# Performance work log

Hardware: AMD Instinct MI355X
Metric: run time of the kernel (lower is better)

Reference implementation:

```python
import jax, jax.numpy as jnp
import numpy as np

N_CLASSES_FG = 20  # n_classes - 1

def _norm(t, axis=1):
    # F.normalize(t, dim=axis, eps=1e-10)
    n = jnp.linalg.norm(t, axis=axis, keepdims=True)
    return t / jnp.maximum(n, 1e-10)

def setup_inputs() -> dict:
    key = jax.random.key(0)
    ks = jax.random.split(key, 6)
    B, C, H, W = 8, 512, 80, 80
    N, Hr, Wr = 100, 40, 40
    return {
        "code_C": jax.random.normal(ks[0], (B, C, H, W), jnp.float32),
        "code_BG": jax.random.normal(ks[1], (B, C, H, W), jnp.float32),
        "ref_code_c": jax.random.normal(ks[2], (N, C, Hr, Wr), jnp.float32),
        "ref_code_bg": jax.random.normal(ks[3], (N, C, Hr, Wr), jnp.float32),
        "sum_patch_coord": jax.random.randint(ks[4], (N, 2), 0, Hr, dtype=jnp.int32),
        "cls_mask": jax.random.randint(ks[5], (N,), 0, N_CLASSES_FG, dtype=jnp.int32),
    }

def reference(code_C, code_BG, ref_code_c, ref_code_bg, sum_patch_coord, cls_mask):
    B, Cdim, H, W = code_C.shape
    N = ref_code_c.shape[0]
    code_C = _norm(code_C)   # channelwise L2 normalize
    code_BG = _norm(code_BG)
    # gather per-annotation feature vectors: ref_code_c[i, :, pc[i,1], pc[i,0]] -> [N, C]
    code_vectors = ref_code_c[jnp.arange(N), :, sum_patch_coord[:, 1], sum_patch_coord[:, 0]]
    # mean-mode prototypes: class-wise mean of gathered vectors
    protos = jax.ops.segment_sum(code_vectors, cls_mask, num_segments=N_CLASSES_FG)  # [V, C]
    counts = jax.ops.segment_sum(jnp.ones((N,), code_vectors.dtype), cls_mask, num_segments=N_CLASSES_FG)
    protos = protos / jnp.maximum(counts, 1.0)[:, None]  # classes with 0 vectors stay zero
    # cosine-similarity maps against normalized prototypes
    prob_C = jnp.einsum('bchw,vc->bvhw', code_C, _norm(protos, axis=1))  # [B, V, H, W]
    # pick the most-background pixel (min of summed class similarity), k=1 topk(-x)
    flat = prob_C.sum(axis=1).reshape(B, -1)  # [B, H*W]
    idx = jnp.argmin(flat, axis=1)
    i_x, i_y = idx // W, idx % W
    min_vec = code_BG[jnp.arange(B), :, i_x, i_y]  # [B, C]
    prob_BG = jnp.einsum('bchw,bc->bhw', code_BG, min_vec)  # [B, H, W]
    probs = jnp.concatenate([prob_BG[:, None], prob_C], axis=1)  # [B, V+1, H, W]
    return jax.nn.softmax(probs, axis=1)
```

## Files before the change

kernel.cpp:

```cpp
#include <hip/hip_runtime.h>
#include <math.h>

#define BB 8
#define CC 512
#define HWSZ 6400
#define NN 100
#define HR 40
#define WR 40
#define VV 20
#define VO 21
#define TPX 128
#define NTILE (HWSZ / TPX)

typedef unsigned long long u64;

__device__ __forceinline__ unsigned mapf(float f) {
    unsigned b = __float_as_uint(f);
    return (b & 0x80000000u) ? ~b : (b | 0x80000000u);
}

__global__ __launch_bounds__(512) void k_protos(const float* __restrict__ refc,
                                                const int* __restrict__ coord,
                                                const int* __restrict__ cls,
                                                float* __restrict__ protosT,
                                                u64* __restrict__ batchMin) {
    const int v = blockIdx.x;
    const int c = threadIdx.x;
    if (v == 0 && c < BB) batchMin[c] = ~0ull;

    float acc = 0.f;
    int cnt = 0;
    for (int n = 0; n < NN; ++n) {
        if (cls[n] == v) {
            int y = coord[2 * n + 1];
            int x = coord[2 * n + 0];
            acc += refc[((size_t)(n * CC + c) * HR + y) * WR + x];
            ++cnt;
        }
    }
    acc /= fmaxf((float)cnt, 1.0f);

    float ss = acc * acc;
    #pragma unroll
    for (int off = 32; off; off >>= 1) ss += __shfl_xor(ss, off);
    __shared__ float sW[8];
    const int wave = c >> 6, lane = c & 63;
    if (lane == 0) sW[wave] = ss;
    __syncthreads();
    float tot = 0.f;
    #pragma unroll
    for (int w = 0; w < 8; ++w) tot += sW[w];
    float scale = 1.0f / fmaxf(sqrtf(tot), 1e-10f);

    protosT[c * VV + v] = acc * scale;
}

__global__ __launch_bounds__(256, 2) void k_probC(const float* __restrict__ codeC,
                                                  const float* __restrict__ protosT,
                                                  float* __restrict__ probC,
                                                  u64* __restrict__ batchMin) {
    __shared__ float red[4 * VO * TPX];
    __shared__ float sScale[TPX];
    __shared__ float sPart[2 * TPX];
    __shared__ u64 sKey[2];

    const int tid  = threadIdx.x;
    const int wave = tid >> 6, lane = tid & 63;
    const int b    = blockIdx.x / NTILE;
    const int tile = blockIdx.x % NTILE;
    const int c0   = __builtin_amdgcn_readfirstlane(wave * 128);

    const float* src = codeC + ((size_t)(b * CC + c0)) * HWSZ + tile * TPX + 2 * lane;
    const float* pt  = protosT + (size_t)c0 * VV;

    float2 d[VV];
    #pragma unroll
    for (int v = 0; v < VV; ++v) d[v] = make_float2(0.f, 0.f);
    float2 ss = make_float2(0.f, 0.f);

    #pragma unroll 8
    for (int c = 0; c < 128; ++c) {
        float2 x = *(const float2*)(src + (size_t)c * HWSZ);
        ss.x = fmaf(x.x, x.x, ss.x);
        ss.y = fmaf(x.y, x.y, ss.y);
        const float* pr = pt + c * VV;
        #pragma unroll
        for (int v = 0; v < VV; ++v) {
            float p = pr[v];
            d[v].x = fmaf(x.x, p, d[v].x);
            d[v].y = fmaf(x.y, p, d[v].y);
        }
    }

    #pragma unroll
    for (int v = 0; v < VV; ++v) {
        red[wave * (VO * TPX) + v * TPX + 2 * lane    ] = d[v].x;
        red[wave * (VO * TPX) + v * TPX + 2 * lane + 1] = d[v].y;
    }
    red[wave * (VO * TPX) + VV * TPX + 2 * lane    ] = ss.x;
    red[wave * (VO * TPX) + VV * TPX + 2 * lane + 1] = ss.y;
    __syncthreads();

    float psum = 0.f;
    for (int q = tid; q < VO * TPX; q += 256) {
        float t = red[q] + red[VO * TPX + q] + red[2 * VO * TPX + q] + red[3 * VO * TPX + q];
        red[q] = t;
        if (q < VV * TPX) psum += t;
    }
    __syncthreads();
    if (tid < TPX) sScale[tid] = 1.0f / fmaxf(sqrtf(red[VV * TPX + tid]), 1e-10f);
    sPart[(tid >> 7) * TPX + (tid & 127)] = psum;
    __syncthreads();

    float* dst = probC + (size_t)b * VV * HWSZ + tile * TPX;
    for (int q = tid; q < VV * TPX; q += 256) {
        int v = q >> 7, px = q & 127;
        dst[(size_t)v * HWSZ + px] = red[q] * sScale[px];
    }

    if (tid < TPX) {
        float total = (sPart[tid] + sPart[TPX + tid]) * sScale[tid];
        u64 key = ((u64)mapf(total) << 32) | (unsigned)(tile * TPX + tid);
        #pragma unroll
        for (int off = 32; off; off >>= 1) {
            u64 o = __shfl_xor(key, off);
            if (o < key) key = o;
        }
        if ((tid & 63) == 0) sKey[tid >> 6] = key;
    }
    __syncthreads();
    if (tid == 0) {
        u64 k = sKey[0] < sKey[1] ? sKey[0] : sKey[1];
        atomicMin(&batchMin[b], k);
    }
}

__global__ __launch_bounds__(512) void k_minvec(const u64* __restrict__ batchMin,
                                                const float* __restrict__ codeBG,
                                                float* __restrict__ minvecN) {
    const int b = blockIdx.x, c = threadIdx.x;
    const int pix = (int)(unsigned)(batchMin[b] & 0xFFFFFFFFull);
    float x = codeBG[(size_t)(b * CC + c) * HWSZ + pix];
    float ss = x * x;
    #pragma unroll
    for (int off = 32; off; off >>= 1) ss += __shfl_xor(ss, off);
    __shared__ float sW[8];
    if ((c & 63) == 0) sW[c >> 6] = ss;
    __syncthreads();
    float tot = 0.f;
    #pragma unroll
    for (int w = 0; w < 8; ++w) tot += sW[w];
    minvecN[b * CC + c] = x * (1.0f / fmaxf(sqrtf(tot), 1e-10f));
}

__global__ __launch_bounds__(256, 2) void k_bg_softmax(const float* __restrict__ codeBG,
                                                       const float* __restrict__ minvecN,
                                                       const float* __restrict__ probC,
                                                       float* __restrict__ out) {
    __shared__ float red2[4 * 2 * TPX];
    __shared__ float sExp[VO * TPX];
    __shared__ float sInv[TPX];

    const int tid  = threadIdx.x;
    const int wave = tid >> 6, lane = tid & 63;
    const int b    = blockIdx.x / NTILE;
    const int tile = blockIdx.x % NTILE;
    const int c0   = __builtin_amdgcn_readfirstlane(wave * 128);

    const float* src = codeBG + ((size_t)(b * CC + c0)) * HWSZ + tile * TPX + 2 * lane;
    const float* mv  = minvecN + b * CC + c0;

    float2 ss = make_float2(0.f, 0.f), dg = make_float2(0.f, 0.f);
    #pragma unroll 8
    for (int c = 0; c < 128; ++c) {
        float2 x = *(const float2*)(src + (size_t)c * HWSZ);
        float m = mv[c];
        ss.x = fmaf(x.x, x.x, ss.x);
        ss.y = fmaf(x.y, x.y, ss.y);
        dg.x = fmaf(x.x, m, dg.x);
        dg.y = fmaf(x.y, m, dg.y);
    }
    red2[wave * (2 * TPX) + 2 * lane    ] = ss.x;
    red2[wave * (2 * TPX) + 2 * lane + 1] = ss.y;
    red2[wave * (2 * TPX) + TPX + 2 * lane    ] = dg.x;
    red2[wave * (2 * TPX) + TPX + 2 * lane + 1] = dg.y;
    __syncthreads();
    {
        int q = tid;
        float t = red2[q] + red2[2 * TPX + q] + red2[4 * TPX + q] + red2[6 * TPX + q];
        red2[q] = t;
    }
    __syncthreads();

    if (tid < TPX) {
        const int px = tid;
        float pbg = red2[TPX + px] * (1.0f / fmaxf(sqrtf(red2[px]), 1e-10f));
        const float* pc = probC + (size_t)b * VV * HWSZ + tile * TPX + px;
        float pv[VO];
        pv[0] = pbg;
        #pragma unroll
        for (int v = 0; v < VV; ++v) pv[v + 1] = pc[(size_t)v * HWSZ];
        float m = pv[0];
        #pragma unroll
        for (int i = 1; i < VO; ++i) m = fmaxf(m, pv[i]);
        float se = 0.f;
        #pragma unroll
        for (int i = 0; i < VO; ++i) {
            float e = __expf(pv[i] - m);
            sExp[i * TPX + px] = e;
            se += e;
        }
        sInv[px] = 1.0f / se;
    }
    __syncthreads();

    float* dst = out + (size_t)b * VO * HWSZ + tile * TPX;
    for (int q = tid; q < VO * TPX; q += 256) {
        int v = q >> 7, px = q & 127;
        dst[(size_t)v * HWSZ + px] = sExp[q] * sInv[px];
    }
}

extern "C" void kernel_launch(void* const* d_in, const int* in_sizes, int n_in,
                              void* d_out, int out_size, void* d_ws, size_t ws_size,
                              hipStream_t stream) {
    const float* codeC  = (const float*)d_in[0];
    const float* codeBG = (const float*)d_in[1];
    const float* refc   = (const float*)d_in[2];
    const int* coord = (const int*)d_in[4];
    const int* cls   = (const int*)d_in[5];
    float* out = (float*)d_out;

    char* ws = (char*)d_ws;
    float* protosT  = (float*)(ws);
    float* probC    = (float*)(ws + 40960);
    float* minvecN  = (float*)(ws + 4136960);
    u64*   batchMin = (u64*)  (ws + 4153344);

    k_protos    <<<dim3(VV),        dim3(512), 0, stream>>>(refc, coord, cls, protosT, batchMin);
    k_probC     <<<dim3(BB * NTILE), dim3(256), 0, stream>>>(codeC, protosT, probC, batchMin);
    k_minvec    <<<dim3(BB),        dim3(512), 0, stream>>>(batchMin, codeBG, minvecN);
    k_bg_softmax<<<dim3(BB * NTILE), dim3(256), 0, stream>>>(codeBG, minvecN, probC, out);
}
```

Measured before the change: 71.07 us.

## Stage channel tiles via async global-to-LDS double buffering with wider pixel tiles

Both heavy kernels now stream input channel blocks of 32 into a double-buffered LDS stage using global_load_lds, prefetching the next block while computing on the current. The pixel tile grows to 256 so each thread handles four pixels with float4 reads. The reduction and softmax epilogues are reorganised so each thread owns a pixel and writes outputs directly. This halves the number of blocks to 200, which may leave CUs idle, and the larger LDS footprint limits occupancy.

New measurement: 91.17 us. 28.3% more time.

```diff
diff --git a/kernel.cpp b/kernel.cpp
--- a/kernel.cpp
+++ b/kernel.cpp
@@ -9,14 +9,22 @@
 #define WR 40
 #define VV 20
 #define VO 21
-#define TPX 128
-#define NTILE (HWSZ / TPX)
+#define TPX 256
+#define NT (HWSZ / TPX)
+#define KB 32
+#define NKB (CC / KB)
 
 typedef unsigned long long u64;
 
 __device__ __forceinline__ unsigned mapf(float f) {
     unsigned b = __float_as_uint(f);
     return (b & 0x80000000u) ? ~b : (b | 0x80000000u);
+}
+
+__device__ __forceinline__ void gload16(const float* gp, const float* lp) {
+    __builtin_amdgcn_global_load_lds(
+        (const __attribute__((address_space(1))) void*)gp,
+        (__attribute__((address_space(3))) void*)lp, 16, 0, 0);
 }
 
 __global__ __launch_bounds__(512) void k_protos(const float* __restrict__ refc,
@@ -59,79 +67,114 @@
                                                   const float* __restrict__ protosT,
                                                   float* __restrict__ probC,
                                                   u64* __restrict__ batchMin) {
-    __shared__ float red[4 * VO * TPX];
-    __shared__ float sScale[TPX];
-    __shared__ float sPart[2 * TPX];
-    __shared__ u64 sKey[2];
+    __shared__ float stage[2][KB * TPX];
+    __shared__ u64 sKey[4];
 
     const int tid  = threadIdx.x;
-    const int wave = tid >> 6, lane = tid & 63;
-    const int b    = blockIdx.x / NTILE;
-    const int tile = blockIdx.x % NTILE;
-    const int c0   = __builtin_amdgcn_readfirstlane(wave * 128);
-
-    const float* src = codeC + ((size_t)(b * CC + c0)) * HWSZ + tile * TPX + 2 * lane;
-    const float* pt  = protosT + (size_t)c0 * VV;
-
-    float2 d[VV];
-    #pragma unroll
-    for (int v = 0; v < VV; ++v) d[v] = make_float2(0.f, 0.f);
-    float2 ss = make_float2(0.f, 0.f);
-
-    #pragma unroll 8
-    for (int c = 0; c < 128; ++c) {
-        float2 x = *(const float2*)(src + (size_t)c * HWSZ);
-        ss.x = fmaf(x.x, x.x, ss.x);
-        ss.y = fmaf(x.y, x.y, ss.y);
-        const float* pr = pt + c * VV;
+    const int w    = tid >> 6, lane = tid & 63;
+    const int b    = blockIdx.x / NT;
+    const int tile = blockIdx.x % NT;
+    const int c0w  = __builtin_amdgcn_readfirstlane(w * 8);
+
+    const float* gbase = codeC + (size_t)b * CC * HWSZ + tile * TPX;
+
+    float d[VV][4];
+    #pragma unroll
+    for (int v = 0; v < VV; ++v) { d[v][0] = d[v][1] = d[v][2] = d[v][3] = 0.f; }
+    float ss0 = 0.f, ss1 = 0.f, ss2 = 0.f, ss3 = 0.f;
+
+    #pragma unroll
+    for (int k = 0; k < 8; ++k) {
+        int r = 4 * k + w;
+        gload16(gbase + (size_t)r * HWSZ + lane * 4, &stage[0][r * TPX]);
+    }
+    __syncthreads();
+
+    int buf = 0;
+    for (int t = 0; t < NKB; ++t) {
+        if (t < NKB - 1) {
+            #pragma unroll
+            for (int k = 0; k < 8; ++k) {
+                int r = 4 * k + w;
+                gload16(gbase + (size_t)((t + 1) * KB + r) * HWSZ + lane * 4,
+                        &stage[buf ^ 1][r * TPX]);
+            }
+        }
+        const float* pt = protosT + (size_t)(t * KB + c0w) * VV;
         #pragma unroll
-        for (int v = 0; v < VV; ++v) {
-            float p = pr[v];
-            d[v].x = fmaf(x.x, p, d[v].x);
-            d[v].y = fmaf(x.y, p, d[v].y);
-        }
-    }
-
-    #pragma unroll
-    for (int v = 0; v < VV; ++v) {
-        red[wave * (VO * TPX) + v * TPX + 2 * lane    ] = d[v].x;
-        red[wave * (VO * TPX) + v * TPX + 2 * lane + 1] = d[v].y;
-    }
-    red[wave * (VO * TPX) + VV * TPX + 2 * lane    ] = ss.x;
-    red[wave * (VO * TPX) + VV * TPX + 2 * lane + 1] = ss.y;
-    __syncthreads();
-
+        for (int j = 0; j < 8; ++j) {
+            float4 x = *(const float4*)&stage[buf][(w * 8 + j) * TPX + lane * 4];
+            ss0 = fmaf(x.x, x.x, ss0);
+            ss1 = fmaf(x.y, x.y, ss1);
+            ss2 = fmaf(x.z, x.z, ss2);
+            ss3 = fmaf(x.w, x.w, ss3);
+            const float* pr = pt + j * VV;
+            #pragma unroll
+            for (int v = 0; v < VV; ++v) {
+                float p = pr[v];
+                d[v][0] = fmaf(x.x, p, d[v][0]);
+                d[v][1] = fmaf(x.y, p, d[v][1]);
+                d[v][2] = fmaf(x.z, p, d[v][2]);
+                d[v][3] = fmaf(x.w, p, d[v][3]);
+            }
+        }
+        __syncthreads();
+        buf ^= 1;
+    }
+
+    float* redA = &stage[0][0];
+    const int px = tid;
+    float* dst = probC + (size_t)b * VV * HWSZ + tile * TPX;
+
+    *(float4*)&redA[(w * 11 + 0) * TPX + lane * 4] = make_float4(ss0, ss1, ss2, ss3);
+    #pragma unroll
+    for (int v = 0; v < 10; ++v)
+        *(float4*)&redA[(w * 11 + 1 + v) * TPX + lane * 4] =
+            make_float4(d[v][0], d[v][1], d[v][2], d[v][3]);
+    __syncthreads();
+
+    float ssT = redA[(0 * 11) * TPX + px] + redA[(1 * 11) * TPX + px] +
+                redA[(2 * 11) * TPX + px] + redA[(3 * 11) * TPX + px];
+    float scale = 1.0f / fmaxf(sqrtf(ssT), 1e-10f);
     float psum = 0.f;
-    for (int q = tid; q < VO * TPX; q += 256) {
-        float t = red[q] + red[VO * TPX + q] + red[2 * VO * TPX + q] + red[3 * VO * TPX + q];
-        red[q] = t;
-        if (q < VV * TPX) psum += t;
-    }
-    __syncthreads();
-    if (tid < TPX) sScale[tid] = 1.0f / fmaxf(sqrtf(red[VV * TPX + tid]), 1e-10f);
-    sPart[(tid >> 7) * TPX + (tid & 127)] = psum;
-    __syncthreads();
-
-    float* dst = probC + (size_t)b * VV * HWSZ + tile * TPX;
-    for (int q = tid; q < VV * TPX; q += 256) {
-        int v = q >> 7, px = q & 127;
-        dst[(size_t)v * HWSZ + px] = red[q] * sScale[px];
-    }
-
-    if (tid < TPX) {
-        float total = (sPart[tid] + sPart[TPX + tid]) * sScale[tid];
-        u64 key = ((u64)mapf(total) << 32) | (unsigned)(tile * TPX + tid);
-        #pragma unroll
-        for (int off = 32; off; off >>= 1) {
-            u64 o = __shfl_xor(key, off);
-            if (o < key) key = o;
-        }
-        if ((tid & 63) == 0) sKey[tid >> 6] = key;
-    }
+    #pragma unroll
+    for (int v = 0; v < 10; ++v) {
+        float dv = redA[(0 * 11 + 1 + v) * TPX + px] + redA[(1 * 11 + 1 + v) * TPX + px] +
+                   redA[(2 * 11 + 1 + v) * TPX + px] + redA[(3 * 11 + 1 + v) * TPX + px];
+        float p = dv * scale;
+        dst[(size_t)v * HWSZ + px] = p;
+        psum += p;
+    }
+    __syncthreads();
+
+    #pragma unroll
+    for (int v = 0; v < 10; ++v)
+        *(float4*)&redA[(w * 11 + v) * TPX + lane * 4] =
+            make_float4(d[10 + v][0], d[10 + v][1], d[10 + v][2], d[10 + v][3]);
+    __syncthreads();
+    #pragma unroll
+    for (int v = 0; v < 10; ++v) {
+        float dv = redA[(0 * 11 + v) * TPX + px] + redA[(1 * 11 + v) * TPX + px] +
+                   redA[(2 * 11 + v) * TPX + px] + redA[(3 * 11 + v) * TPX + px];
+        float p = dv * scale;
+        dst[(size_t)(10 + v) * HWSZ + px] = p;
+        psum += p;
+    }
+
+    u64 key = ((u64)mapf(psum) << 32) | (unsigned)(tile * TPX + px);
+    #pragma unroll
+    for (int off = 32; off; off >>= 1) {
+        u64 o = __shfl_xor(key, off);
+        if (o < key) key = o;
+    }
+    if (lane == 0) sKey[w] = key;
     __syncthreads();
     if (tid == 0) {
-        u64 k = sKey[0] < sKey[1] ? sKey[0] : sKey[1];
-        atomicMin(&batchMin[b], k);
+        u64 kk = sKey[0];
+        kk = sKey[1] < kk ? sKey[1] : kk;
+        kk = sKey[2] < kk ? sKey[2] : kk;
+        kk = sKey[3] < kk ? sKey[3] : kk;
+        atomicMin(&batchMin[b], kk);
     }
 }
 
@@ -157,68 +200,81 @@
                                                        const float* __restrict__ minvecN,
                                                        const float* __restrict__ probC,
                                                        float* __restrict__ out) {
-    __shared__ float red2[4 * 2 * TPX];
-    __shared__ float sExp[VO * TPX];
-    __shared__ float sInv[TPX];
+    __shared__ float stage[2][KB * TPX];
+    __shared__ float redB[8 * TPX];
 
     const int tid  = threadIdx.x;
-    const int wave = tid >> 6, lane = tid & 63;
-    const int b    = blockIdx.x / NTILE;
-    const int tile = blockIdx.x % NTILE;
-    const int c0   = __builtin_amdgcn_readfirstlane(wave * 128);
-
-    const float* src = codeBG + ((size_t)(b * CC + c0)) * HWSZ + tile * TPX + 2 * lane;
-    const float* mv  = minvecN + b * CC + c0;
-
-    float2 ss = make_float2(0.f, 0.f), dg = make_float2(0.f, 0.f);
-    #pragma unroll 8
-    for (int c = 0; c < 128; ++c) {
-        float2 x = *(const float2*)(src + (size_t)c * HWSZ);
-        float m = mv[c];
-        ss.x = fmaf(x.x, x.x, ss.x);
-        ss.y = fmaf(x.y, x.y, ss.y);
-        dg.x = fmaf(x.x, m, dg.x);
-        dg.y = fmaf(x.y, m, dg.y);
-    }
-    red2[wave * (2 * TPX) + 2 * lane    ] = ss.x;
-    red2[wave * (2 * TPX) + 2 * lane + 1] = ss.y;
-    red2[wave * (2 * TPX) + TPX + 2 * lane    ] = dg.x;
-    red2[wave * (2 * TPX) + TPX + 2 * lane + 1] = dg.y;
-    __syncthreads();
-    {
-        int q = tid;
-        float t = red2[q] + red2[2 * TPX + q] + red2[4 * TPX + q] + red2[6 * TPX + q];
-        red2[q] = t;
-    }
-    __syncthreads();
-
-    if (tid < TPX) {
-        const int px = tid;
-        float pbg = red2[TPX + px] * (1.0f / fmaxf(sqrtf(red2[px]), 1e-10f));
-        const float* pc = probC + (size_t)b * VV * HWSZ + tile * TPX + px;
-        float pv[VO];
-        pv[0] = pbg;
+    const int w    = tid >> 6, lane = tid & 63;
+    const int b    = blockIdx.x / NT;
+    const int tile = blockIdx.x % NT;
+    const int c0w  = __builtin_amdgcn_readfirstlane(w * 8);
+
+    const float* gbase = codeBG + (size_t)b * CC * HWSZ + tile * TPX;
+
+    float ss0 = 0.f, ss1 = 0.f, ss2 = 0.f, ss3 = 0.f;
+    float dg0 = 0.f, dg1 = 0.f, dg2 = 0.f, dg3 = 0.f;
+
+    #pragma unroll
+    for (int k = 0; k < 8; ++k) {
+        int r = 4 * k + w;
+        gload16(gbase + (size_t)r * HWSZ + lane * 4, &stage[0][r * TPX]);
+    }
+    __syncthreads();
+
+    int buf = 0;
+    for (int t = 0; t < NKB; ++t) {
+        if (t < NKB - 1) {
+            #pragma unroll
+            for (int k = 0; k < 8; ++k) {
+                int r = 4 * k + w;
+                gload16(gbase + (size_t)((t + 1) * KB + r) * HWSZ + lane * 4,
+                        &stage[buf ^ 1][r * TPX]);
+            }
+        }
+        const float* mv = minvecN + b * CC + t * KB + c0w;
         #pragma unroll
-        for (int v = 0; v < VV; ++v) pv[v + 1] = pc[(size_t)v * HWSZ];
-        float m = pv[0];
-        #pragma unroll
-        for (int i = 1; i < VO; ++i) m = fmaxf(m, pv[i]);
-        float se = 0.f;
-        #pragma unroll
-        for (int i = 0; i < VO; ++i) {
-            float e = __expf(pv[i] - m);
-            sExp[i * TPX + px] = e;
-            se += e;
-        }
-        sInv[px] = 1.0f / se;
-    }
-    __syncthreads();
-
-    float* dst = out + (size_t)b * VO * HWSZ + tile * TPX;
-    for (int q = tid; q < VO * TPX; q += 256) {
-        int v = q >> 7, px = q & 127;
-        dst[(size_t)v * HWSZ + px] = sExp[q] * sInv[px];
-    }
+        for (int j = 0; j < 8; ++j) {
+            float4 x = *(const float4*)&stage[buf][(w * 8 + j) * TPX + lane * 4];
+            float m = mv[j];
+            ss0 = fmaf(x.x, x.x, ss0);
+            ss1 = fmaf(x.y, x.y, ss1);
+            ss2 = fmaf(x.z, x.z, ss2);
+            ss3 = fmaf(x.w, x.w, ss3);
+            dg0 = fmaf(x.x, m, dg0);
+            dg1 = fmaf(x.y, m, dg1);
+            dg2 = fmaf(x.z, m, dg2);
+            dg3 = fmaf(x.w, m, dg3);
+        }
+        __syncthreads();
+        buf ^= 1;
+    }
+
+    *(float4*)&redB[(w * 2 + 0) * TPX + lane * 4] = make_float4(ss0, ss1, ss2, ss3);
+    *(float4*)&redB[(w * 2 + 1) * TPX + lane * 4] = make_float4(dg0, dg1, dg2, dg3);
+    __syncthreads();
+
+    const int px = tid;
+    float ssT = redB[0 * TPX + px] + redB[2 * TPX + px] + redB[4 * TPX + px] + redB[6 * TPX + px];
+    float dgT = redB[1 * TPX + px] + redB[3 * TPX + px] + redB[5 * TPX + px] + redB[7 * TPX + px];
+    float pbg = dgT * (1.0f / fmaxf(sqrtf(ssT), 1e-10f));
+
+    float pv[VO];
+    pv[0] = pbg;
+    const float* pc = probC + (size_t)b * VV * HWSZ + tile * TPX + px;
+    #pragma unroll
+    for (int v = 0; v < VV; ++v) pv[v + 1] = pc[(size_t)v * HWSZ];
+
+    float m = pv[0];
+    #pragma unroll
+    for (int i = 1; i < VO; ++i) m = fmaxf(m, pv[i]);
+    float se = 0.f;
+    #pragma unroll
+    for (int i = 0; i < VO; ++i) { pv[i] = __expf(pv[i] - m); se += pv[i]; }
+    float inv = 1.0f / se;
+
+    float* dstp = out + (size_t)b * VO * HWSZ + tile * TPX + px;
+    #pragma unroll
+    for (int i = 0; i < VO; ++i) dstp[(size_t)i * HWSZ] = pv[i] * inv;
 }
 
 extern "C" void kernel_launch(void* const* d_in, const int* in_sizes, int n_in,
@@ -237,8 +293,8 @@
     float* minvecN  = (float*)(ws + 4136960);
     u64*   batchMin = (u64*)  (ws + 4153344);
 
-    k_protos    <<<dim3(VV),        dim3(512), 0, stream>>>(refc, coord, cls, protosT, batchMin);
-    k_probC     <<<dim3(BB * NTILE), dim3(256), 0, stream>>>(codeC, protosT, probC, batchMin);
-    k_minvec    <<<dim3(BB),        dim3(512), 0, stream>>>(batchMin, codeBG, minvecN);
-    k_bg_softmax<<<dim3(BB * NTILE), dim3(256), 0, stream>>>(codeBG, minvecN, probC, out);
-}
+    k_protos    <<<dim3(VV),      dim3(512), 0, stream>>>(refc, coord, cls, protosT, batchMin);
+    k_probC     <<<dim3(BB * NT), dim3(256), 0, stream>>>(codeC, protosT, probC, batchMin);
+    k_minvec    <<<dim3(BB),      dim3(512), 0, stream>>>(batchMin, codeBG, minvecN);
+    k_bg_softmax<<<dim3(BB * NT), dim3(256), 0, stream>>>(codeBG, minvecN, probC, out);
+}
```

## Split channel reduction across blocks with float4 loads and separate finish kernels

Applied to the files above, without the earlier changes.

Doubles the pixel tile to 256 and has each thread load float4 instead of float2. The 512 channels are split into two blocks per tile that write partial sums to workspace, and two new finish kernels combine the partials, normalize, then run the argmin and softmax steps. The aim is wider memory transactions and more independent blocks for the bandwidth-bound channel reductions. In exchange it adds two kernel launches and extra global traffic for the partials, and the float4 accumulators raise register pressure.

Result: faster. 67.60 us (-4.9%).

```diff
diff --git a/kernel.cpp b/kernel.cpp
--- a/kernel.cpp
+++ b/kernel.cpp
@@ -9,8 +9,8 @@
 #define WR 40
 #define VV 20
 #define VO 21
-#define TPX 128
-#define NTILE (HWSZ / TPX)
+#define TPX 256
+#define NT (HWSZ / TPX)
 
 typedef unsigned long long u64;
 
@@ -55,83 +55,106 @@
     protosT[c * VV + v] = acc * scale;
 }
 
-__global__ __launch_bounds__(256, 2) void k_probC(const float* __restrict__ codeC,
-                                                  const float* __restrict__ protosT,
-                                                  float* __restrict__ probC,
-                                                  u64* __restrict__ batchMin) {
-    __shared__ float red[4 * VO * TPX];
-    __shared__ float sScale[TPX];
-    __shared__ float sPart[2 * TPX];
-    __shared__ u64 sKey[2];
-
-    const int tid  = threadIdx.x;
-    const int wave = tid >> 6, lane = tid & 63;
-    const int b    = blockIdx.x / NTILE;
-    const int tile = blockIdx.x % NTILE;
-    const int c0   = __builtin_amdgcn_readfirstlane(wave * 128);
-
-    const float* src = codeC + ((size_t)(b * CC + c0)) * HWSZ + tile * TPX + 2 * lane;
+__global__ __launch_bounds__(256) void k_probC_part(const float* __restrict__ codeC,
+                                                    const float* __restrict__ protosT,
+                                                    float* __restrict__ partC) {
+    __shared__ float red[4 * 11 * TPX];
+
+    const int tid  = threadIdx.x;
+    const int w    = tid >> 6, lane = tid & 63;
+    const int blk  = blockIdx.x;
+    const int cg   = blk & 1;
+    const int tile = (blk >> 1) % NT;
+    const int b    = blk / (2 * NT);
+    const int c0   = __builtin_amdgcn_readfirstlane(cg * 256 + w * 64);
+
+    const float* src = codeC + ((size_t)(b * CC + c0)) * HWSZ + tile * TPX + 4 * lane;
     const float* pt  = protosT + (size_t)c0 * VV;
 
-    float2 d[VV];
-    #pragma unroll
-    for (int v = 0; v < VV; ++v) d[v] = make_float2(0.f, 0.f);
-    float2 ss = make_float2(0.f, 0.f);
+    float4 d[VV];
+    #pragma unroll
+    for (int v = 0; v < VV; ++v) d[v] = make_float4(0.f, 0.f, 0.f, 0.f);
+    float4 ss = make_float4(0.f, 0.f, 0.f, 0.f);
 
     #pragma unroll 8
-    for (int c = 0; c < 128; ++c) {
-        float2 x = *(const float2*)(src + (size_t)c * HWSZ);
+    for (int c = 0; c < 64; ++c) {
+        float4 x = *(const float4*)(src + (size_t)c * HWSZ);
         ss.x = fmaf(x.x, x.x, ss.x);
         ss.y = fmaf(x.y, x.y, ss.y);
+        ss.z = fmaf(x.z, x.z, ss.z);
+        ss.w = fmaf(x.w, x.w, ss.w);
         const float* pr = pt + c * VV;
         #pragma unroll
         for (int v = 0; v < VV; ++v) {
             float p = pr[v];
             d[v].x = fmaf(x.x, p, d[v].x);
             d[v].y = fmaf(x.y, p, d[v].y);
+            d[v].z = fmaf(x.z, p, d[v].z);
+            d[v].w = fmaf(x.w, p, d[v].w);
         }
     }
 
+    float* dstp = partC + (size_t)blk * (VO * TPX);
+
+    *(float4*)&red[(w * 11 + 0) * TPX + 4 * lane] = ss;
+    #pragma unroll
+    for (int r = 0; r < 10; ++r)
+        *(float4*)&red[(w * 11 + 1 + r) * TPX + 4 * lane] = d[r];
+    __syncthreads();
+    for (int q = tid; q < 11 * TPX; q += 256) {
+        float t = red[q] + red[11 * TPX + q] + red[22 * TPX + q] + red[33 * TPX + q];
+        dstp[q] = t;
+    }
+    __syncthreads();
+
+    #pragma unroll
+    for (int r = 0; r < 10; ++r)
+        *(float4*)&red[(w * 11 + r) * TPX + 4 * lane] = d[10 + r];
+    __syncthreads();
+    for (int q = tid; q < 10 * TPX; q += 256) {
+        float t = red[q] + red[11 * TPX + q] + red[22 * TPX + q] + red[33 * TPX + q];
+        dstp[11 * TPX + q] = t;
+    }
+}
+
+__global__ __launch_bounds__(256) void k_finishC(const float* __restrict__ partC,
+                                                 float* __restrict__ probC,
+                                                 u64* __restrict__ batchMin) {
+    __shared__ u64 sKey[4];
+    const int tid  = threadIdx.x;
+    const int tile = blockIdx.x % NT;
+    const int b    = blockIdx.x / NT;
+
+    const float* p0 = partC + ((size_t)(b * 2 * NT + tile * 2)) * (VO * TPX);
+    const float* p1 = p0 + VO * TPX;
+
+    float ssT = p0[tid] + p1[tid];
+    float scale = 1.0f / fmaxf(sqrtf(ssT), 1e-10f);
+
+    float psum = 0.f;
+    float* dst = probC + (size_t)b * VV * HWSZ + tile * TPX;
     #pragma unroll
     for (int v = 0; v < VV; ++v) {
-        red[wave * (VO * TPX) + v * TPX + 2 * lane    ] = d[v].x;
-        red[wave * (VO * TPX) + v * TPX + 2 * lane + 1] = d[v].y;
-    }
-    red[wave * (VO * TPX) + VV * TPX + 2 * lane    ] = ss.x;
-    red[wave * (VO * TPX) + VV * TPX + 2 * lane + 1] = ss.y;
-    __syncthreads();
-
-    float psum = 0.f;
-    for (int q = tid; q < VO * TPX; q += 256) {
-        float t = red[q] + red[VO * TPX + q] + red[2 * VO * TPX + q] + red[3 * VO * TPX + q];
-        red[q] = t;
-        if (q < VV * TPX) psum += t;
-    }
-    __syncthreads();
-    if (tid < TPX) sScale[tid] = 1.0f / fmaxf(sqrtf(red[VV * TPX + tid]), 1e-10f);
-    sPart[(tid >> 7) * TPX + (tid & 127)] = psum;
-    __syncthreads();
-
-    float* dst = probC + (size_t)b * VV * HWSZ + tile * TPX;
-    for (int q = tid; q < VV * TPX; q += 256) {
-        int v = q >> 7, px = q & 127;
-        dst[(size_t)v * HWSZ + px] = red[q] * sScale[px];
-    }
-
-    if (tid < TPX) {
-        float total = (sPart[tid] + sPart[TPX + tid]) * sScale[tid];
-        u64 key = ((u64)mapf(total) << 32) | (unsigned)(tile * TPX + tid);
-        #pragma unroll
-        for (int off = 32; off; off >>= 1) {
-            u64 o = __shfl_xor(key, off);
-            if (o < key) key = o;
-        }
-        if ((tid & 63) == 0) sKey[tid >> 6] = key;
-    }
+        float dv = p0[(1 + v) * TPX + tid] + p1[(1 + v) * TPX + tid];
+        float pv = dv * scale;
+        dst[(size_t)v * HWSZ + tid] = pv;
+        psum += pv;
+    }
+
+    u64 key = ((u64)mapf(psum) << 32) | (unsigned)(tile * TPX + tid);
+    #pragma unroll
+    for (int off = 32; off; off >>= 1) {
+        u64 o = __shfl_xor(key, off);
+        if (o < key) key = o;
+    }
+    if ((tid & 63) == 0) sKey[tid >> 6] = key;
     __syncthreads();
     if (tid == 0) {
-        u64 k = sKey[0] < sKey[1] ? sKey[0] : sKey[1];
-        atomicMin(&batchMin[b], k);
+        u64 kk = sKey[0];
+        kk = sKey[1] < kk ? sKey[1] : kk;
+        kk = sKey[2] < kk ? sKey[2] : kk;
+        kk = sKey[3] < kk ? sKey[3] : kk;
+        atomicMin(&batchMin[b], kk);
     }
 }
 
@@ -153,72 +176,81 @@
     minvecN[b * CC + c] = x * (1.0f / fmaxf(sqrtf(tot), 1e-10f));
 }
 
-__global__ __launch_bounds__(256, 2) void k_bg_softmax(const float* __restrict__ codeBG,
-                                                       const float* __restrict__ minvecN,
-                                                       const float* __restrict__ probC,
-                                                       float* __restrict__ out) {
-    __shared__ float red2[4 * 2 * TPX];
-    __shared__ float sExp[VO * TPX];
-    __shared__ float sInv[TPX];
-
-    const int tid  = threadIdx.x;
-    const int wave = tid >> 6, lane = tid & 63;
-    const int b    = blockIdx.x / NTILE;
-    const int tile = blockIdx.x % NTILE;
-    const int c0   = __builtin_amdgcn_readfirstlane(wave * 128);
-
-    const float* src = codeBG + ((size_t)(b * CC + c0)) * HWSZ + tile * TPX + 2 * lane;
+__global__ __launch_bounds__(256) void k_bg_part(const float* __restrict__ codeBG,
+                                                 const float* __restrict__ minvecN,
+                                                 float* __restrict__ partBG) {
+    __shared__ float red[4 * 2 * TPX];
+
+    const int tid  = threadIdx.x;
+    const int w    = tid >> 6, lane = tid & 63;
+    const int blk  = blockIdx.x;
+    const int cg   = blk & 1;
+    const int tile = (blk >> 1) % NT;
+    const int b    = blk / (2 * NT);
+    const int c0   = __builtin_amdgcn_readfirstlane(cg * 256 + w * 64);
+
+    const float* src = codeBG + ((size_t)(b * CC + c0)) * HWSZ + tile * TPX + 4 * lane;
     const float* mv  = minvecN + b * CC + c0;
 
-    float2 ss = make_float2(0.f, 0.f), dg = make_float2(0.f, 0.f);
+    float4 ss = make_float4(0.f, 0.f, 0.f, 0.f);
+    float4 dg = make_float4(0.f, 0.f, 0.f, 0.f);
+
     #pragma unroll 8
-    for (int c = 0; c < 128; ++c) {
-        float2 x = *(const float2*)(src + (size_t)c * HWSZ);
+    for (int c = 0; c < 64; ++c) {
+        float4 x = *(const float4*)(src + (size_t)c * HWSZ);
         float m = mv[c];
         ss.x = fmaf(x.x, x.x, ss.x);
         ss.y = fmaf(x.y, x.y, ss.y);
+        ss.z = fmaf(x.z, x.z, ss.z);
+        ss.w = fmaf(x.w, x.w, ss.w);
         dg.x = fmaf(x.x, m, dg.x);
         dg.y = fmaf(x.y, m, dg.y);
-    }
-    red2[wave * (2 * TPX) + 2 * lane    ] = ss.x;
-    red2[wave * (2 * TPX) + 2 * lane + 1] = ss.y;
-    red2[wave * (2 * TPX) + TPX + 2 * lane    ] = dg.x;
-    red2[wave * (2 * TPX) + TPX + 2 * lane + 1] = dg.y;
-    __syncthreads();
-    {
-        int q = tid;
-        float t = red2[q] + red2[2 * TPX + q] + red2[4 * TPX + q] + red2[6 * TPX + q];
-        red2[q] = t;
-    }
-    __syncthreads();
-
-    if (tid < TPX) {
-        const int px = tid;
-        float pbg = red2[TPX + px] * (1.0f / fmaxf(sqrtf(red2[px]), 1e-10f));
-        const float* pc = probC + (size_t)b * VV * HWSZ + tile * TPX + px;
-        float pv[VO];
-        pv[0] = pbg;
-        #pragma unroll
-        for (int v = 0; v < VV; ++v) pv[v + 1] = pc[(size_t)v * HWSZ];
-        float m = pv[0];
-        #pragma unroll
-        for (int i = 1; i < VO; ++i) m = fmaxf(m, pv[i]);
-        float se = 0.f;
-        #pragma unroll
-        for (int i = 0; i < VO; ++i) {
-            float e = __expf(pv[i] - m);
-            sExp[i * TPX + px] = e;
-            se += e;
-        }
-        sInv[px] = 1.0f / se;
-    }
-    __syncthreads();
-
-    float* dst = out + (size_t)b * VO * HWSZ + tile * TPX;
-    for (int q = tid; q < VO * TPX; q += 256) {
-        int v = q >> 7, px = q & 127;
-        dst[(size_t)v * HWSZ + px] = sExp[q] * sInv[px];
-    }
+        dg.z = fmaf(x.z, m, dg.z);
+        dg.w = fmaf(x.w, m, dg.w);
+    }
+
+    *(float4*)&red[(w * 2 + 0) * TPX + 4 * lane] = ss;
+    *(float4*)&red[(w * 2 + 1) * TPX + 4 * lane] = dg;
+    __syncthreads();
+
+    float* dstp = partBG + (size_t)blk * (2 * TPX);
+    for (int q = tid; q < 2 * TPX; q += 256) {
+        float t = red[q] + red[2 * TPX + q] + red[4 * TPX + q] + red[6 * TPX + q];
+        dstp[q] = t;
+    }
+}
+
+__global__ __launch_bounds__(256) void k_finishBG(const float* __restrict__ partBG,
+                                                  const float* __restrict__ probC,
+                                                  float* __restrict__ out) {
+    const int tid  = threadIdx.x;
+    const int tile = blockIdx.x % NT;
+    const int b    = blockIdx.x / NT;
+
+    const float* q0 = partBG + ((size_t)(b * 2 * NT + tile * 2)) * (2 * TPX);
+    const float* q1 = q0 + 2 * TPX;
+
+    float ssT = q0[tid] + q1[tid];
+    float dgT = q0[TPX + tid] + q1[TPX + tid];
+    float pbg = dgT * (1.0f / fmaxf(sqrtf(ssT), 1e-10f));
+
+    float pv[VO];
+    pv[0] = pbg;
+    const float* pc = probC + (size_t)b * VV * HWSZ + tile * TPX + tid;
+    #pragma unroll
+    for (int v = 0; v < VV; ++v) pv[v + 1] = pc[(size_t)v * HWSZ];
+
+    float m = pv[0];
+    #pragma unroll
+    for (int i = 1; i < VO; ++i) m = fmaxf(m, pv[i]);
+    float se = 0.f;
+    #pragma unroll
+    for (int i = 0; i < VO; ++i) { pv[i] = __expf(pv[i] - m); se += pv[i]; }
+    float inv = 1.0f / se;
+
+    float* dstp = out + (size_t)b * VO * HWSZ + tile * TPX + tid;
+    #pragma unroll
+    for (int i = 0; i < VO; ++i) dstp[(size_t)i * HWSZ] = pv[i] * inv;
 }
 
 extern "C" void kernel_launch(void* const* d_in, const int* in_sizes, int n_in,
@@ -236,9 +268,13 @@
     float* probC    = (float*)(ws + 40960);
     float* minvecN  = (float*)(ws + 4136960);
     u64*   batchMin = (u64*)  (ws + 4153344);
-
-    k_protos    <<<dim3(VV),        dim3(512), 0, stream>>>(refc, coord, cls, protosT, batchMin);
-    k_probC     <<<dim3(BB * NTILE), dim3(256), 0, stream>>>(codeC, protosT, probC, batchMin);
-    k_minvec    <<<dim3(BB),        dim3(512), 0, stream>>>(batchMin, codeBG, minvecN);
-    k_bg_softmax<<<dim3(BB * NTILE), dim3(256), 0, stream>>>(codeBG, minvecN, probC, out);
-}
+    float* partC    = (float*)(ws + 4153408);
+    float* partBG   = (float*)(ws + 12755008);
+
+    k_protos    <<<dim3(VV),          dim3(512), 0, stream>>>(refc, coord, cls, protosT, batchMin);
+    k_probC_part<<<dim3(BB * NT * 2), dim3(256), 0, stream>>>(codeC, protosT, partC);
+    k_finishC   <<<dim3(BB * NT),     dim3(256), 0, stream>>>(partC, probC, batchMin);
+    k_minvec    <<<dim3(BB),          dim3(512), 0, stream>>>(batchMin, codeBG, minvecN);
+    k_bg_part   <<<dim3(BB * NT * 2), dim3(256), 0, stream>>>(codeBG, minvecN, partBG);
+    k_finishBG  <<<dim3(BB * NT),     dim3(256), 0, stream>>>(partBG, probC, out);
+}
```

## Fuse min-vector kernel into probC via last-block counter; write softmax directly

Applied to the files above, without the earlier changes.

Removes the separate k_minvec launch. An atomic per-batch counter lets the last finishing probC block gather and normalize the background min vector. The softmax kernel now writes outputs straight from registers instead of staging them through shared memory. Other changes: reductions use vectorized float2 stores, loops unroll to 16, and the min-occupancy launch bound hint is dropped. This saves one launch and some LDS traffic, at the cost of threadfence/atomic serialization and a serial tail in the last block.

After: 91.36 us. 28.6% more time.

```diff
diff --git a/kernel.cpp b/kernel.cpp
--- a/kernel.cpp
+++ b/kernel.cpp
@@ -10,7 +10,7 @@
 #define VV 20
 #define VO 21
 #define TPX 128
-#define NTILE (HWSZ / TPX)
+#define NT (HWSZ / TPX)
 
 typedef unsigned long long u64;
 
@@ -23,22 +23,23 @@
                                                 const int* __restrict__ coord,
                                                 const int* __restrict__ cls,
                                                 float* __restrict__ protosT,
-                                                u64* __restrict__ batchMin) {
+                                                u64* __restrict__ batchMin,
+                                                unsigned* __restrict__ cnt) {
     const int v = blockIdx.x;
     const int c = threadIdx.x;
-    if (v == 0 && c < BB) batchMin[c] = ~0ull;
+    if (v == 0 && c < BB) { batchMin[c] = ~0ull; cnt[c] = 0u; }
 
     float acc = 0.f;
-    int cnt = 0;
+    int n_in_cls = 0;
     for (int n = 0; n < NN; ++n) {
         if (cls[n] == v) {
             int y = coord[2 * n + 1];
             int x = coord[2 * n + 0];
             acc += refc[((size_t)(n * CC + c) * HR + y) * WR + x];
-            ++cnt;
-        }
-    }
-    acc /= fmaxf((float)cnt, 1.0f);
+            ++n_in_cls;
+        }
+    }
+    acc /= fmaxf((float)n_in_cls, 1.0f);
 
     float ss = acc * acc;
     #pragma unroll
@@ -55,20 +56,25 @@
     protosT[c * VV + v] = acc * scale;
 }
 
-__global__ __launch_bounds__(256, 2) void k_probC(const float* __restrict__ codeC,
-                                                  const float* __restrict__ protosT,
-                                                  float* __restrict__ probC,
-                                                  u64* __restrict__ batchMin) {
-    __shared__ float red[4 * VO * TPX];
+__global__ __launch_bounds__(256) void k_probC(const float* __restrict__ codeC,
+                                               const float* __restrict__ codeBG,
+                                               const float* __restrict__ protosT,
+                                               float* __restrict__ probC,
+                                               u64* __restrict__ batchMin,
+                                               unsigned* __restrict__ cnt,
+                                               float* __restrict__ minvecN) {
+    __shared__ float red[4 * 21 * TPX];
     __shared__ float sScale[TPX];
-    __shared__ float sPart[2 * TPX];
     __shared__ u64 sKey[2];
+    __shared__ int sLast;
+    __shared__ unsigned sPix;
+    __shared__ float sR[4];
 
     const int tid  = threadIdx.x;
-    const int wave = tid >> 6, lane = tid & 63;
-    const int b    = blockIdx.x / NTILE;
-    const int tile = blockIdx.x % NTILE;
-    const int c0   = __builtin_amdgcn_readfirstlane(wave * 128);
+    const int w    = tid >> 6, lane = tid & 63;
+    const int b    = blockIdx.x / NT;
+    const int tile = blockIdx.x % NT;
+    const int c0   = __builtin_amdgcn_readfirstlane(w * 128);
 
     const float* src = codeC + ((size_t)(b * CC + c0)) * HWSZ + tile * TPX + 2 * lane;
     const float* pt  = protosT + (size_t)c0 * VV;
@@ -78,12 +84,12 @@
     for (int v = 0; v < VV; ++v) d[v] = make_float2(0.f, 0.f);
     float2 ss = make_float2(0.f, 0.f);
 
-    #pragma unroll 8
-    for (int c = 0; c < 128; ++c) {
-        float2 x = *(const float2*)(src + (size_t)c * HWSZ);
+    #pragma unroll 16
+    for (int i = 0; i < 128; ++i) {
+        float2 x = *(const float2*)(src + (size_t)i * HWSZ);
         ss.x = fmaf(x.x, x.x, ss.x);
         ss.y = fmaf(x.y, x.y, ss.y);
-        const float* pr = pt + c * VV;
+        const float* pr = pt + i * VV;
         #pragma unroll
         for (int v = 0; v < VV; ++v) {
             float p = pr[v];
@@ -92,98 +98,98 @@
         }
     }
 
-    #pragma unroll
-    for (int v = 0; v < VV; ++v) {
-        red[wave * (VO * TPX) + v * TPX + 2 * lane    ] = d[v].x;
-        red[wave * (VO * TPX) + v * TPX + 2 * lane + 1] = d[v].y;
-    }
-    red[wave * (VO * TPX) + VV * TPX + 2 * lane    ] = ss.x;
-    red[wave * (VO * TPX) + VV * TPX + 2 * lane + 1] = ss.y;
-    __syncthreads();
-
-    float psum = 0.f;
-    for (int q = tid; q < VO * TPX; q += 256) {
-        float t = red[q] + red[VO * TPX + q] + red[2 * VO * TPX + q] + red[3 * VO * TPX + q];
+    *(float2*)&red[(w * 21 + 0) * TPX + 2 * lane] = ss;
+    #pragma unroll
+    for (int v = 0; v < VV; ++v)
+        *(float2*)&red[(w * 21 + 1 + v) * TPX + 2 * lane] = d[v];
+    __syncthreads();
+
+    for (int q = tid; q < 21 * TPX; q += 256) {
+        float t = red[q] + red[21 * TPX + q] + red[42 * TPX + q] + red[63 * TPX + q];
         red[q] = t;
-        if (q < VV * TPX) psum += t;
-    }
-    __syncthreads();
-    if (tid < TPX) sScale[tid] = 1.0f / fmaxf(sqrtf(red[VV * TPX + tid]), 1e-10f);
-    sPart[(tid >> 7) * TPX + (tid & 127)] = psum;
+    }
+    __syncthreads();
+    if (tid < TPX) sScale[tid] = 1.0f / fmaxf(sqrtf(red[tid]), 1e-10f);
     __syncthreads();
 
     float* dst = probC + (size_t)b * VV * HWSZ + tile * TPX;
     for (int q = tid; q < VV * TPX; q += 256) {
-        int v = q >> 7, px = q & 127;
-        dst[(size_t)v * HWSZ + px] = red[q] * sScale[px];
+        int v = q >> 7, px = q & (TPX - 1);
+        dst[(size_t)v * HWSZ + px] = red[TPX + q] * sScale[px];
     }
 
     if (tid < TPX) {
-        float total = (sPart[tid] + sPart[TPX + tid]) * sScale[tid];
-        u64 key = ((u64)mapf(total) << 32) | (unsigned)(tile * TPX + tid);
+        float psum = 0.f;
+        #pragma unroll
+        for (int v = 0; v < VV; ++v) psum += red[(1 + v) * TPX + tid];
+        psum *= sScale[tid];
+        u64 key = ((u64)mapf(psum) << 32) | (unsigned)(tile * TPX + tid);
         #pragma unroll
         for (int off = 32; off; off >>= 1) {
             u64 o = __shfl_xor(key, off);
             if (o < key) key = o;
         }
-        if ((tid & 63) == 0) sKey[tid >> 6] = key;
+        if (lane == 0) sKey[w] = key;
     }
     __syncthreads();
     if (tid == 0) {
-        u64 k = sKey[0] < sKey[1] ? sKey[0] : sKey[1];
-        atomicMin(&batchMin[b], k);
-    }
-}
-
-__global__ __launch_bounds__(512) void k_minvec(const u64* __restrict__ batchMin,
-                                                const float* __restrict__ codeBG,
-                                                float* __restrict__ minvecN) {
-    const int b = blockIdx.x, c = threadIdx.x;
-    const int pix = (int)(unsigned)(batchMin[b] & 0xFFFFFFFFull);
-    float x = codeBG[(size_t)(b * CC + c) * HWSZ + pix];
-    float ss = x * x;
-    #pragma unroll
-    for (int off = 32; off; off >>= 1) ss += __shfl_xor(ss, off);
-    __shared__ float sW[8];
-    if ((c & 63) == 0) sW[c >> 6] = ss;
-    __syncthreads();
-    float tot = 0.f;
-    #pragma unroll
-    for (int w = 0; w < 8; ++w) tot += sW[w];
-    minvecN[b * CC + c] = x * (1.0f / fmaxf(sqrtf(tot), 1e-10f));
-}
-
-__global__ __launch_bounds__(256, 2) void k_bg_softmax(const float* __restrict__ codeBG,
-                                                       const float* __restrict__ minvecN,
-                                                       const float* __restrict__ probC,
-                                                       float* __restrict__ out) {
+        u64 kk = sKey[0] < sKey[1] ? sKey[0] : sKey[1];
+        atomicMin(&batchMin[b], kk);
+        __threadfence();
+        unsigned old = atomicAdd(&cnt[b], 1u);
+        sLast = (old == NT - 1) ? 1 : 0;
+    }
+    __syncthreads();
+
+    if (sLast) {
+        if (tid == 0) {
+            __threadfence();
+            u64 kk = atomicMin(&batchMin[b], ~0ull);
+            sPix = (unsigned)(kk & 0xFFFFFFFFull);
+        }
+        __syncthreads();
+        const int pix = (int)sPix;
+        float x0 = codeBG[((size_t)(b * CC + tid)) * HWSZ + pix];
+        float x1 = codeBG[((size_t)(b * CC + 256 + tid)) * HWSZ + pix];
+        float s2 = fmaf(x0, x0, x1 * x1);
+        #pragma unroll
+        for (int off = 32; off; off >>= 1) s2 += __shfl_xor(s2, off);
+        if (lane == 0) sR[w] = s2;
+        __syncthreads();
+        float totq = sR[0] + sR[1] + sR[2] + sR[3];
+        float sc = 1.0f / fmaxf(sqrtf(totq), 1e-10f);
+        minvecN[b * CC + tid] = x0 * sc;
+        minvecN[b * CC + 256 + tid] = x1 * sc;
+    }
+}
+
+__global__ __launch_bounds__(256) void k_bg_softmax(const float* __restrict__ codeBG,
+                                                    const float* __restrict__ minvecN,
+                                                    const float* __restrict__ probC,
+                                                    float* __restrict__ out) {
     __shared__ float red2[4 * 2 * TPX];
-    __shared__ float sExp[VO * TPX];
-    __shared__ float sInv[TPX];
 
     const int tid  = threadIdx.x;
-    const int wave = tid >> 6, lane = tid & 63;
-    const int b    = blockIdx.x / NTILE;
-    const int tile = blockIdx.x % NTILE;
-    const int c0   = __builtin_amdgcn_readfirstlane(wave * 128);
+    const int w    = tid >> 6, lane = tid & 63;
+    const int b    = blockIdx.x / NT;
+    const int tile = blockIdx.x % NT;
+    const int c0   = __builtin_amdgcn_readfirstlane(w * 128);
 
     const float* src = codeBG + ((size_t)(b * CC + c0)) * HWSZ + tile * TPX + 2 * lane;
     const float* mv  = minvecN + b * CC + c0;
 
     float2 ss = make_float2(0.f, 0.f), dg = make_float2(0.f, 0.f);
-    #pragma unroll 8
-    for (int c = 0; c < 128; ++c) {
-        float2 x = *(const float2*)(src + (size_t)c * HWSZ);
-        float m = mv[c];
+    #pragma unroll 16
+    for (int i = 0; i < 128; ++i) {
+        float2 x = *(const float2*)(src + (size_t)i * HWSZ);
+        float m = mv[i];
         ss.x = fmaf(x.x, x.x, ss.x);
         ss.y = fmaf(x.y, x.y, ss.y);
         dg.x = fmaf(x.x, m, dg.x);
         dg.y = fmaf(x.y, m, dg.y);
     }
-    red2[wave * (2 * TPX) + 2 * lane    ] = ss.x;
-    red2[wave * (2 * TPX) + 2 * lane + 1] = ss.y;
-    red2[wave * (2 * TPX) + TPX + 2 * lane    ] = dg.x;
-    red2[wave * (2 * TPX) + TPX + 2 * lane + 1] = dg.y;
+    *(float2*)&red2[(w * 2 + 0) * TPX + 2 * lane] = ss;
+    *(float2*)&red2[(w * 2 + 1) * TPX + 2 * lane] = dg;
     __syncthreads();
     {
         int q = tid;
@@ -195,29 +201,24 @@
     if (tid < TPX) {
         const int px = tid;
         float pbg = red2[TPX + px] * (1.0f / fmaxf(sqrtf(red2[px]), 1e-10f));
-        const float* pc = probC + (size_t)b * VV * HWSZ + tile * TPX + px;
+
         float pv[VO];
         pv[0] = pbg;
+        const float* pc = probC + (size_t)b * VV * HWSZ + tile * TPX + px;
         #pragma unroll
         for (int v = 0; v < VV; ++v) pv[v + 1] = pc[(size_t)v * HWSZ];
+
         float m = pv[0];
         #pragma unroll
         for (int i = 1; i < VO; ++i) m = fmaxf(m, pv[i]);
         float se = 0.f;
         #pragma unroll
-        for (int i = 0; i < VO; ++i) {
-            float e = __expf(pv[i] - m);
-            sExp[i * TPX + px] = e;
-            se += e;
-        }
-        sInv[px] = 1.0f / se;
-    }
-    __syncthreads();
-
-    float* dst = out + (size_t)b * VO * HWSZ + tile * TPX;
-    for (int q = tid; q < VO * TPX; q += 256) {
-        int v = q >> 7, px = q & 127;
-        dst[(size_t)v * HWSZ + px] = sExp[q] * sInv[px];
+        for (int i = 0; i < VO; ++i) { pv[i] = __expf(pv[i] - m); se += pv[i]; }
+        float inv = 1.0f / se;
+
+        float* dstp = out + (size_t)b * VO * HWSZ + tile * TPX + px;
+        #pragma unroll
+        for (int i = 0; i < VO; ++i) dstp[(size_t)i * HWSZ] = pv[i] * inv;
     }
 }
 
@@ -232,13 +233,13 @@
     float* out = (float*)d_out;
 
     char* ws = (char*)d_ws;
-    float* protosT  = (float*)(ws);
-    float* probC    = (float*)(ws + 40960);
-    float* minvecN  = (float*)(ws + 4136960);
-    u64*   batchMin = (u64*)  (ws + 4153344);
-
-    k_protos    <<<dim3(VV),        dim3(512), 0, stream>>>(refc, coord, cls, protosT, batchMin);
-    k_probC     <<<dim3(BB * NTILE), dim3(256), 0, stream>>>(codeC, protosT, probC, batchMin);
-    k_minvec    <<<dim3(BB),        dim3(512), 0, stream>>>(batchMin, codeBG, minvecN);
-    k_bg_softmax<<<dim3(BB * NTILE), dim3(256), 0, stream>>>(codeBG, minvecN, probC, out);
-}
+    float*    protosT  = (float*)   (ws);
+    float*    probC    = (float*)   (ws + 40960);
+    float*    minvecN  = (float*)   (ws + 4136960);
+    u64*      batchMin = (u64*)     (ws + 4153344);
+    unsigned* cnt      = (unsigned*)(ws + 4153408);
+
+    k_protos    <<<dim3(VV),      dim3(512), 0, stream>>>(refc, coord, cls, protosT, batchMin, cnt);
+    k_probC     <<<dim3(BB * NT), dim3(256), 0, stream>>>(codeC, codeBG, protosT, probC, batchMin, cnt, minvecN);
+    k_bg_softmax<<<dim3(BB * NT), dim3(256), 0, stream>>>(codeBG, minvecN, probC, out);
+}
```
